# Performance work log

Measured on AMD Instinct MI355X. Metric: run time of the kernel, lower is better.

## Reference

```python
import jax, jax.numpy as jnp
import numpy as np

SPATIAL = (128, 128)
FFT_SIZE = (256, 256)  # 2 * spatial per dim
FFT_AXES = (-2, -1)


def setup_inputs() -> dict:
    key = jax.random.key(0)
    k1, k2, k3, k4 = jax.random.split(key, 4)
    B, C = 4, 256
    u = jax.random.normal(k1, (B, C, *SPATIAL), dtype=jnp.float32)
    k = jax.random.normal(k2, (C, 64, 64), dtype=jnp.float32)
    pregate = jax.random.uniform(k3, (B, C, *SPATIAL), dtype=jnp.float32)
    postgate = jax.random.uniform(k4, (B, C, *SPATIAL), dtype=jnp.float32)
    return {"u": u, "k": k, "pregate": pregate, "postgate": postgate}


def reference(u, k, pregate, postgate):
    # y = crop(IRFFT(RFFT(u * pregate) * RFFT(k))) * postgate
    u_work = u.astype(jnp.float32) * pregate.astype(jnp.float32)
    u_f = jnp.fft.rfftn(u_work, s=FFT_SIZE, axes=FFT_AXES)      # (B,C,256,129) complex
    k_f = jnp.fft.rfftn(k.astype(jnp.float32), s=FFT_SIZE, axes=FFT_AXES)  # (C,256,129)
    y_f = u_f * k_f[None]
    y = jnp.fft.irfftn(y_f, s=FFT_SIZE, axes=FFT_AXES)          # (B,C,256,256)
    H, W = u.shape[-2], u.shape[-1]
    y = y[..., :H, :W]
    y = y * postgate.astype(jnp.float32)
    return y.astype(u.dtype)
```

## Files before the change

### kernel.cpp

```cpp
#include <hip/hip_runtime.h>


typedef unsigned int uint32;
typedef short short8 __attribute__((ext_vector_type(8)));
typedef float float4v __attribute__((ext_vector_type(4)));
typedef uint32 uint4v __attribute__((ext_vector_type(4)));

__device__ __forceinline__ unsigned short f2bf(float f) {
    uint32 x = __float_as_uint(f);
    uint32 r = (x + 0x7fffu + ((x >> 16) & 1u)) >> 16;
    return (unsigned short)r;
}

#define XLS_BYTES (128 * 192 * 2)
#define KPAD_BYTES (94 * 72 * 2)
#define SMEM_BYTES (XLS_BYTES + KPAD_BYTES)

__global__ __launch_bounds__(256, 2)
void conv_mfma3(const float* __restrict__ u, const float* __restrict__ kk,
                const float* __restrict__ pregate, const float* __restrict__ postgate,
                float* __restrict__ out)
{
    extern __shared__ char smem[];
    unsigned short (*xls)[192]  = (unsigned short(*)[192])smem;
    unsigned short (*kpad)[72]  = (unsigned short(*)[72])(smem + XLS_BYTES);

    const int img = blockIdx.x;
    const int c   = img & 255;
    const int tid = threadIdx.x;

    const float* uimg = u        + (size_t)img * (128*128);
    const float* pimg = pregate  + (size_t)img * (128*128);
    const float* gimg = postgate + (size_t)img * (128*128);
    float*       oimg = out      + (size_t)img * (128*128);
    const float* kimg = kk       + (size_t)c   * (64*64);

    {
        uint4 z = make_uint4(0u,0u,0u,0u);
        uint4* kp4 = (uint4*)&kpad[0][0];
        for (int t = tid; t < KPAD_BYTES/16; t += 256) kp4[t] = z;
    }
    {
        uint4 z = make_uint4(0u,0u,0u,0u);
        for (int t = tid; t < 128*8; t += 256) {
            int r = t >> 3, c8 = 128 + ((t & 7) << 3);
            *(uint4*)&xls[r][c8] = z;
        }
    }
    for (int t = tid; t < 128*16; t += 256) {
        int r = t >> 4, c8 = (t & 15) << 3;
        const float4 u0 = *(const float4*)(uimg + r*128 + c8);
        const float4 u1 = *(const float4*)(uimg + r*128 + c8 + 4);
        const float4 p0 = *(const float4*)(pimg + r*128 + c8);
        const float4 p1 = *(const float4*)(pimg + r*128 + c8 + 4);
        unsigned short h0 = f2bf(u0.x*p0.x), h1 = f2bf(u0.y*p0.y);
        unsigned short h2 = f2bf(u0.z*p0.z), h3 = f2bf(u0.w*p0.w);
        unsigned short h4 = f2bf(u1.x*p1.x), h5 = f2bf(u1.y*p1.y);
        unsigned short h6 = f2bf(u1.z*p1.z), h7 = f2bf(u1.w*p1.w);
        uint4 w;
        w.x = (uint32)h7 | ((uint32)h6 << 16);
        w.y = (uint32)h5 | ((uint32)h4 << 16);
        w.z = (uint32)h3 | ((uint32)h2 << 16);
        w.w = (uint32)h1 | ((uint32)h0 << 16);
        *(uint4*)&xls[r][120 - c8] = w;
    }
    for (int t = tid; t < 64*16; t += 256) {
        int p = t >> 4, c4 = (t & 15) << 2;
        const float4 kv = *(const float4*)(kimg + p*64 + c4);
        uint2 w;
        w.x = (uint32)f2bf(kv.x) | ((uint32)f2bf(kv.y) << 16);
        w.y = (uint32)f2bf(kv.z) | ((uint32)f2bf(kv.w) << 16);
        *(uint2*)&kpad[15 + p][c4] = w;
    }
    __syncthreads();

    const int wv   = tid >> 6;
    const int lane = tid & 63;
    const int jh = wv & 1;
    const int ih = ((wv >> 1) ^ ((blockIdx.x >> 8) & 1)) & 1;
    const int J0 = jh << 6, I0 = ih << 6;
    const int m    = lane & 15;
    const int quad = lane >> 4;

    float4v acc[4][4] = {};

    const int rlo = (I0 - 63 > 0) ? I0 - 63 : 0;
    const int rhi = (I0 + 63 < 127) ? I0 + 63 : 127;

    const int cbase = 127 - J0 - m + 8*quad;
    const uint32 sh = (uint32)((cbase & 1) << 4);
    const int dws0  = (cbase - 48) >> 1;

    const uint32* xls32 = (const uint32*)smem;

#pragma unroll 1
    for (int r = rlo; r <= rhi; ++r) {
        const uint32* row32 = xls32 + r*96 + dws0;
        uint32 dw[6][5];
#pragma unroll
        for (int s = 0; s < 6; ++s) {
            const uint32* p = row32 + 8*s;
            dw[s][0] = p[0]; dw[s][1] = p[1]; dw[s][2] = p[2];
            dw[s][3] = p[3]; dw[s][4] = p[4];
        }
        short8 av[6];
#pragma unroll
        for (int s = 0; s < 6; ++s) {
            uint4v f;
            f.x = __builtin_amdgcn_alignbit(dw[s][1], dw[s][0], sh);
            f.y = __builtin_amdgcn_alignbit(dw[s][2], dw[s][1], sh);
            f.z = __builtin_amdgcn_alignbit(dw[s][3], dw[s][2], sh);
            f.w = __builtin_amdgcn_alignbit(dw[s][4], dw[s][3], sh);
            av[s] = __builtin_bit_cast(short8, f);
        }

        const int t0 = 15 + I0 + m - r;
#pragma unroll
        for (int q1 = 0; q1 < 2; ++q1) {
#pragma unroll
            for (int nt = 0; nt < 4; ++nt) {
                int p15 = t0 + 16*nt;
                p15 = p15 < 0 ? 0 : (p15 > 93 ? 93 : p15);
                const short8 bv = *(const short8*)&kpad[p15][32*q1 + 8*quad];
                acc[0][nt] = __builtin_amdgcn_mfma_f32_16x16x32_bf16(av[3 + 2*q1], bv, acc[0][nt], 0,0,0);
                acc[1][nt] = __builtin_amdgcn_mfma_f32_16x16x32_bf16(av[2 + 2*q1], bv, acc[1][nt], 0,0,0);
                acc[2][nt] = __builtin_amdgcn_mfma_f32_16x16x32_bf16(av[1 + 2*q1], bv, acc[2][nt], 0,0,0);
                acc[3][nt] = __builtin_amdgcn_mfma_f32_16x16x32_bf16(av[0 + 2*q1], bv, acc[3][nt], 0,0,0);
            }
        }
    }

    __syncthreads();
    float (*bufE)[132] = (float(*)[132])smem;
    for (int h = 0; h < 2; ++h) {
        if (ih == h) {
#pragma unroll
            for (int mt = 0; mt < 4; ++mt)
#pragma unroll
                for (int nt = 0; nt < 4; ++nt)
#pragma unroll
                    for (int rg = 0; rg < 4; ++rg) {
                        int iloc = 16*nt + m;
                        int j    = J0 + 16*mt + 4*quad + rg;
                        bufE[iloc][j] = acc[mt][nt][rg];
                    }
        }
        __syncthreads();
#pragma unroll 1
        for (int s = 0; s < 8; ++s) {
            int chunk = (s << 8) + tid;
            int row = chunk >> 5, c4 = (chunk & 31) << 2;
            float4 v = *(float4*)&bufE[row][c4];
            int gi = (h << 6) + row;
            const float4 g = *(const float4*)(gimg + gi*128 + c4);
            float4 o;
            o.x = v.x*g.x; o.y = v.y*g.y; o.z = v.z*g.z; o.w = v.w*g.w;
            *(float4*)(oimg + gi*128 + c4) = o;
        }
        __syncthreads();
    }
}

extern "C" void kernel_launch(void* const* d_in, const int* in_sizes, int n_in,
                              void* d_out, int out_size, void* d_ws, size_t ws_size,
                              hipStream_t stream) {
    const float* u    = (const float*)d_in[0];
    const float* k    = (const float*)d_in[1];
    const float* pre  = (const float*)d_in[2];
    const float* post = (const float*)d_in[3];
    float* out = (float*)d_out;

    conv_mfma3<<<dim3(1024), dim3(256), SMEM_BYTES, stream>>>(u, k, pre, post, out);
}
```

Before: 360.7 us.

## Interleave wave output tiles and skip zero kernel blocks in direct bf16 MFMA convolution

The per-wave output tiling changes from contiguous 64x64 quadrants to interleaved 16-wide strips, so every wave covers rows and columns across the whole image. Kernel rows are loaded unclamped and only zero-padded by one row. Whole MFMA n-tiles are skipped when the input row falls outside their kernel support, and kernel column blocks that lie entirely in the zero band are no longer multiplied. Shared memory shrinks with a narrower input pitch and smaller kernel pad, and launch bounds are raised to 3 blocks per CU for more occupancy. The cost is extra branching in the inner loop and a possible change in register pressure under the tighter launch bounds.

Measured after the change: 329.9 us. 8.5% less time.

```diff
diff --git a/kernel.cpp b/kernel.cpp
--- a/kernel.cpp
+++ b/kernel.cpp
@@ -12,18 +12,19 @@
     return (unsigned short)r;
 }
 
-#define XLS_BYTES (128 * 192 * 2)
-#define KPAD_BYTES (94 * 72 * 2)
+#define XLS_PITCH 160
+#define XLS_BYTES (128 * XLS_PITCH * 2)
+#define KPAD_BYTES (65 * 72 * 2)
 #define SMEM_BYTES (XLS_BYTES + KPAD_BYTES)
 
-__global__ __launch_bounds__(256, 2)
-void conv_mfma3(const float* __restrict__ u, const float* __restrict__ kk,
+__global__ __launch_bounds__(256, 3)
+void conv_mfma4(const float* __restrict__ u, const float* __restrict__ kk,
                 const float* __restrict__ pregate, const float* __restrict__ postgate,
                 float* __restrict__ out)
 {
     extern __shared__ char smem[];
-    unsigned short (*xls)[192]  = (unsigned short(*)[192])smem;
-    unsigned short (*kpad)[72]  = (unsigned short(*)[72])(smem + XLS_BYTES);
+    unsigned short (*xls)[XLS_PITCH] = (unsigned short(*)[XLS_PITCH])smem;
+    unsigned short (*kpad)[72] = (unsigned short(*)[72])(smem + XLS_BYTES);
 
     const int img = blockIdx.x;
     const int c   = img & 255;
@@ -35,17 +36,11 @@
     float*       oimg = out      + (size_t)img * (128*128);
     const float* kimg = kk       + (size_t)c   * (64*64);
 
-    {
-        uint4 z = make_uint4(0u,0u,0u,0u);
-        uint4* kp4 = (uint4*)&kpad[0][0];
-        for (int t = tid; t < KPAD_BYTES/16; t += 256) kp4[t] = z;
-    }
-    {
-        uint4 z = make_uint4(0u,0u,0u,0u);
-        for (int t = tid; t < 128*8; t += 256) {
-            int r = t >> 3, c8 = 128 + ((t & 7) << 3);
-            *(uint4*)&xls[r][c8] = z;
-        }
+    const uint4 z = make_uint4(0u,0u,0u,0u);
+    if (tid < 9) ((uint4*)&kpad[0][0])[tid] = z;
+    for (int t = tid; t < 512; t += 256) {
+        int r = t >> 2, cc = 128 + ((t & 3) << 3);
+        *(uint4*)&xls[r][cc] = z;
     }
     for (int t = tid; t < 128*16; t += 256) {
         int r = t >> 4, c8 = (t & 15) << 3;
@@ -70,80 +65,81 @@
         uint2 w;
         w.x = (uint32)f2bf(kv.x) | ((uint32)f2bf(kv.y) << 16);
         w.y = (uint32)f2bf(kv.z) | ((uint32)f2bf(kv.w) << 16);
-        *(uint2*)&kpad[15 + p][c4] = w;
+        *(uint2*)&kpad[1 + p][c4] = w;
     }
     __syncthreads();
 
     const int wv   = tid >> 6;
     const int lane = tid & 63;
-    const int jh = wv & 1;
-    const int ih = ((wv >> 1) ^ ((blockIdx.x >> 8) & 1)) & 1;
-    const int J0 = jh << 6, I0 = ih << 6;
+    const int jw = wv >> 1;
+    const int iw = (wv & 1) ^ ((blockIdx.x >> 8) & 1);
     const int m    = lane & 15;
     const int quad = lane >> 4;
+    const int i16  = iw << 4;
+
+    const int c0    = 127 - (jw << 4) - m + (quad << 3);
+    const uint32 sh = (uint32)((c0 & 1) << 4);
+    const int bw3   = (c0 >> 1) - 48;
+    const int rhi   = 111 + i16;
+
+    const uint32* xls32 = (const uint32*)smem;
 
     float4v acc[4][4] = {};
 
-    const int rlo = (I0 - 63 > 0) ? I0 - 63 : 0;
-    const int rhi = (I0 + 63 < 127) ? I0 + 63 : 127;
-
-    const int cbase = 127 - J0 - m + 8*quad;
-    const uint32 sh = (uint32)((cbase & 1) << 4);
-    const int dws0  = (cbase - 48) >> 1;
-
-    const uint32* xls32 = (const uint32*)smem;
-
 #pragma unroll 1
-    for (int r = rlo; r <= rhi; ++r) {
-        const uint32* row32 = xls32 + r*96 + dws0;
-        uint32 dw[6][5];
+    for (int r = 0; r <= rhi; ++r) {
+        const uint32* row32 = xls32 + r*80 + bw3;
+        uint32 dw[4][5];
 #pragma unroll
-        for (int s = 0; s < 6; ++s) {
-            const uint32* p = row32 + 8*s;
-            dw[s][0] = p[0]; dw[s][1] = p[1]; dw[s][2] = p[2];
-            dw[s][3] = p[3]; dw[s][4] = p[4];
+        for (int w = 0; w < 4; ++w) {
+            const int O = (3 - w) << 4;
+            dw[w][0] = row32[O+0]; dw[w][1] = row32[O+1];
+            dw[w][2] = row32[O+2]; dw[w][3] = row32[O+3];
+            dw[w][4] = row32[O+4];
         }
-        short8 av[6];
+        short8 av[4];
 #pragma unroll
-        for (int s = 0; s < 6; ++s) {
+        for (int w = 0; w < 4; ++w) {
             uint4v f;
-            f.x = __builtin_amdgcn_alignbit(dw[s][1], dw[s][0], sh);
-            f.y = __builtin_amdgcn_alignbit(dw[s][2], dw[s][1], sh);
-            f.z = __builtin_amdgcn_alignbit(dw[s][3], dw[s][2], sh);
-            f.w = __builtin_amdgcn_alignbit(dw[s][4], dw[s][3], sh);
-            av[s] = __builtin_bit_cast(short8, f);
+            f.x = __builtin_amdgcn_alignbit(dw[w][1], dw[w][0], sh);
+            f.y = __builtin_amdgcn_alignbit(dw[w][2], dw[w][1], sh);
+            f.z = __builtin_amdgcn_alignbit(dw[w][3], dw[w][2], sh);
+            f.w = __builtin_amdgcn_alignbit(dw[w][4], dw[w][3], sh);
+            av[w] = __builtin_bit_cast(short8, f);
         }
 
-        const int t0 = 15 + I0 + m - r;
+        const int t0 = i16 + m - r;
 #pragma unroll
-        for (int q1 = 0; q1 < 2; ++q1) {
-#pragma unroll
-            for (int nt = 0; nt < 4; ++nt) {
-                int p15 = t0 + 16*nt;
-                p15 = p15 < 0 ? 0 : (p15 > 93 ? 93 : p15);
-                const short8 bv = *(const short8*)&kpad[p15][32*q1 + 8*quad];
-                acc[0][nt] = __builtin_amdgcn_mfma_f32_16x16x32_bf16(av[3 + 2*q1], bv, acc[0][nt], 0,0,0);
-                acc[1][nt] = __builtin_amdgcn_mfma_f32_16x16x32_bf16(av[2 + 2*q1], bv, acc[1][nt], 0,0,0);
-                acc[2][nt] = __builtin_amdgcn_mfma_f32_16x16x32_bf16(av[1 + 2*q1], bv, acc[2][nt], 0,0,0);
-                acc[3][nt] = __builtin_amdgcn_mfma_f32_16x16x32_bf16(av[0 + 2*q1], bv, acc[3][nt], 0,0,0);
-            }
+        for (int nt = 0; nt < 4; ++nt) {
+            const int nb = (nt << 5) + i16;
+            if (r < nb - 63 || r > nb + 15) continue;
+            const int p   = t0 + (nt << 5);
+            const int row = ((uint32)p < 64u) ? (p + 1) : 0;
+            const short8 bv0 = *(const short8*)&kpad[row][quad << 3];
+            const short8 bv1 = *(const short8*)&kpad[row][32 + (quad << 3)];
+            acc[0][nt] = __builtin_amdgcn_mfma_f32_16x16x32_bf16(av[0], bv0, acc[0][nt], 0,0,0);
+            acc[1][nt] = __builtin_amdgcn_mfma_f32_16x16x32_bf16(av[1], bv0, acc[1][nt], 0,0,0);
+            acc[2][nt] = __builtin_amdgcn_mfma_f32_16x16x32_bf16(av[2], bv0, acc[2][nt], 0,0,0);
+            acc[3][nt] = __builtin_amdgcn_mfma_f32_16x16x32_bf16(av[3], bv0, acc[3][nt], 0,0,0);
+            acc[1][nt] = __builtin_amdgcn_mfma_f32_16x16x32_bf16(av[0], bv1, acc[1][nt], 0,0,0);
+            acc[2][nt] = __builtin_amdgcn_mfma_f32_16x16x32_bf16(av[1], bv1, acc[2][nt], 0,0,0);
+            acc[3][nt] = __builtin_amdgcn_mfma_f32_16x16x32_bf16(av[2], bv1, acc[3][nt], 0,0,0);
         }
     }
 
     __syncthreads();
     float (*bufE)[132] = (float(*)[132])smem;
+#pragma unroll
     for (int h = 0; h < 2; ++h) {
-        if (ih == h) {
+#pragma unroll
+        for (int ntl = 0; ntl < 2; ++ntl) {
+            const int iloc = (ntl << 5) + i16 + m;
 #pragma unroll
             for (int mt = 0; mt < 4; ++mt)
 #pragma unroll
-                for (int nt = 0; nt < 4; ++nt)
-#pragma unroll
-                    for (int rg = 0; rg < 4; ++rg) {
-                        int iloc = 16*nt + m;
-                        int j    = J0 + 16*mt + 4*quad + rg;
-                        bufE[iloc][j] = acc[mt][nt][rg];
-                    }
+                for (int rg = 0; rg < 4; ++rg)
+                    bufE[iloc][(mt << 5) + (jw << 4) + (quad << 2) + rg] =
+                        acc[mt][(h << 1) + ntl][rg];
         }
         __syncthreads();
 #pragma unroll 1
@@ -170,5 +166,5 @@
     const float* post = (const float*)d_in[3];
     float* out = (float*)d_out;
 
-    conv_mfma3<<<dim3(1024), dim3(256), SMEM_BYTES, stream>>>(u, k, pre, post, out);
+    conv_mfma4<<<dim3(1024), dim3(256), SMEM_BYTES, stream>>>(u, k, pre, post, out);
 }
```
